# Kernel optimization log

Hardware: AMD Instinct MI355X
Metric: run time of the kernel (lower is better)

The kernel has to match this reference:

```python
import jax, jax.numpy as jnp
import numpy as np

B, L, N, DOUT = 8, 8192, 256, 256  # batch, seq_len, state_dim, output_dim


def setup_inputs() -> dict:
    key = jax.random.key(0)
    k_u, k_h, k_w = jax.random.split(key, 3)
    u = jax.random.normal(k_u, (B, L, 1), dtype=jnp.float32)
    # impulse response buffer (stands in for A_bar^i @ B_bar rows); decay-scaled for realism
    h = jax.random.normal(k_h, (L, N), dtype=jnp.float32) * 0.02
    W = jax.random.normal(k_w, (DOUT, N), dtype=jnp.float32) * (1.0 / np.sqrt(N))
    return {"u": u, "h": h, "W": W}


def reference(u, h, W):
    L_ = h.shape[0]
    n_fft = 2 * L_
    # FFT-based long convolution: U:[B, n_fft//2+1, 1], H:[n_fft//2+1, N]
    U = jnp.fft.rfft(u, n=n_fft, axis=1)
    H = jnp.fft.rfft(h, n=n_fft, axis=0)
    M = U * H[None, :, :]                      # broadcast channel 1 -> N
    m = jnp.fft.irfft(M, n=n_fft, axis=1)[:, :L_, :]  # [B, L, N]
    return jnp.einsum('bln,on->blo', m, W)     # Linear(state_dim -> output_dim), no bias
```

## Files before the change

kernel.cpp:

```cpp
#include <hip/hip_runtime.h>
#include <hip/hip_bf16.h>
#include <stdint.h>
#include <stddef.h>

typedef __attribute__((ext_vector_type(4))) float f32x4;
typedef __attribute__((ext_vector_type(8))) short s16x8;

#define B_    8
#define L_    8192
#define N_    256
#define DOUT_ 256

__device__ __forceinline__ unsigned short f2bf(float f) {
  unsigned int x = __float_as_uint(f);
  x += 0x7fff + ((x >> 16) & 1);
  return (unsigned short)(x >> 16);
}

__global__ void k_convert(const float* __restrict__ h, const float* __restrict__ W,
                          unsigned short* __restrict__ hb, unsigned short* __restrict__ Wb) {
  int t = blockIdx.x * 256 + threadIdx.x;
  int base = t * 4;
  const int TH = L_ * N_;
  const int TW = DOUT_ * N_;
  if (base < TH) {
    float4 v = *(const float4*)(h + base);
    hb[base + 0] = f2bf(v.x); hb[base + 1] = f2bf(v.y);
    hb[base + 2] = f2bf(v.z); hb[base + 3] = f2bf(v.w);
  } else if (base < TH + TW) {
    int wb = base - TH;
    float4 v = *(const float4*)(W + wb);
    Wb[wb + 0] = f2bf(v.x); Wb[wb + 1] = f2bf(v.y);
    Wb[wb + 2] = f2bf(v.z); Wb[wb + 3] = f2bf(v.w);
  }
}

__global__ void k_amat(const float* __restrict__ u, unsigned short* __restrict__ Am) {
  int t = blockIdx.x * 256 + threadIdx.x;
  int i0 = (t & 15) * 8;
  int lp = (t >> 4) & 127;
  int d  = (t >> 11) & 63;
  int b  = t >> 17;
  const float* ub = u + b * L_;
  int base = 128 * d + lp - i0;
  s16x8 v;
#pragma unroll
  for (int j = 0; j < 8; ++j) {
    int idx = base - j;
    float f = (idx >= 0) ? ub[idx] : 0.0f;
    v[j] = (short)f2bf(f);
  }
  *(s16x8*)(Am + (size_t)t * 8) = v;
}

__global__ void k_gt(const unsigned short* __restrict__ Wb, const unsigned short* __restrict__ hb,
                     unsigned short* __restrict__ gT) {
  int gid  = blockIdx.x * 256 + threadIdx.x;
  int lane = gid & 63;
  int wid  = gid >> 6;
  int o_t  = wid >> 7;
  int i_t  = wid & 127;
  int o0 = o_t * 16, i0 = i_t * 64;
  int ln = lane & 15, hi = lane >> 4;
  f32x4 acc[4] = {};
#pragma unroll
  for (int k0 = 0; k0 < N_; k0 += 32) {
    s16x8 a = *(const s16x8*)(Wb + (o0 + ln) * N_ + k0 + 8 * hi);
#pragma unroll
    for (int ns = 0; ns < 4; ++ns) {
      s16x8 bfr = *(const s16x8*)(hb + (i0 + 16 * ns + ln) * N_ + k0 + 8 * hi);
      acc[ns] = __builtin_amdgcn_mfma_f32_16x16x32_bf16(a, bfr, acc[ns], 0, 0, 0);
    }
  }
#pragma unroll
  for (int ns = 0; ns < 4; ++ns)
#pragma unroll
    for (int q = 0; q < 4; ++q)
      gT[(size_t)(o0 + 4 * hi + q) * L_ + i0 + 16 * ns + ln] = f2bf(acc[ns][q]);
}

__global__ __launch_bounds__(256) void k_main(const unsigned short* __restrict__ Am,
                                              const unsigned short* __restrict__ gT,
                                              float* __restrict__ out) {
  __shared__ short Abuf[128 * 64];
  __shared__ short Bbuf[128 * 64];
  const int c = blockIdx.x;
  const int b = blockIdx.y;
  const int r = 63 - blockIdx.z;
  const int t = threadIdx.x;
  const int lane = t & 63;
  const int w = t >> 6;
  const int wm = (w >> 1) * 64, wn = (w & 1) * 64;
  const int ln = lane & 15, hi = lane >> 4;
  const int ob = c * 128;
  const int trow = t >> 3;
  const int tcol = (t & 7) * 8;
  f32x4 acc[4][4] = {};

  const int nkt = 2 * (r + 1);
  for (int kt = 0; kt < nkt; ++kt) {
    const int i0   = kt * 64;
    const int d    = r - (kt >> 1);
    const int ioff = (kt & 1) * 64;
    const unsigned short* Asrc = Am + (((size_t)(b * 64 + d)) << 14) + ioff + tcol;
    const unsigned short* Bsrc = gT + (size_t)(ob + trow) * L_ + i0 + tcol;
#pragma unroll
    for (int call = 0; call < 4; ++call) {
      __builtin_amdgcn_global_load_lds(
          (const __attribute__((address_space(1))) void*)(Asrc + (size_t)(call * 32 + trow) * 128),
          (__attribute__((address_space(3))) void*)(Abuf + call * 2048 + t * 8),
          16, 0, 0);
    }
#pragma unroll
    for (int call = 0; call < 4; ++call) {
      __builtin_amdgcn_global_load_lds(
          (const __attribute__((address_space(1))) void*)(Bsrc + (size_t)(call * 32) * L_),
          (__attribute__((address_space(3))) void*)(Bbuf + call * 2048 + t * 8),
          16, 0, 0);
    }
    __syncthreads();
#pragma unroll
    for (int k0 = 0; k0 < 64; k0 += 32) {
      s16x8 af[4], bfr[4];
#pragma unroll
      for (int m = 0; m < 4; ++m)
        af[m] = *(const s16x8*)(Abuf + (wm + m * 16 + ln) * 64 + k0 + 8 * hi);
#pragma unroll
      for (int n = 0; n < 4; ++n)
        bfr[n] = *(const s16x8*)(Bbuf + (wn + n * 16 + ln) * 64 + k0 + 8 * hi);
#pragma unroll
      for (int m = 0; m < 4; ++m)
#pragma unroll
        for (int n = 0; n < 4; ++n)
          acc[m][n] = __builtin_amdgcn_mfma_f32_16x16x32_bf16(af[m], bfr[n], acc[m][n], 0, 0, 0);
    }
    __syncthreads();
  }

  const int lb = r * 128;
#pragma unroll
  for (int m = 0; m < 4; ++m)
#pragma unroll
    for (int n = 0; n < 4; ++n)
#pragma unroll
      for (int q = 0; q < 4; ++q) {
        int l = lb + wm + m * 16 + 4 * hi + q;
        int o = ob + wn + n * 16 + ln;
        out[(size_t)(b * L_ + l) * DOUT_ + o] = acc[m][n][q];
      }
}

extern "C" void kernel_launch(void* const* d_in, const int* in_sizes, int n_in,
                              void* d_out, int out_size, void* d_ws, size_t ws_size,
                              hipStream_t stream) {
  const float* u = (const float*)d_in[0];
  const float* h = (const float*)d_in[1];
  const float* W = (const float*)d_in[2];
  float* out = (float*)d_out;

  char* ws = (char*)d_ws;
  unsigned short* hb = (unsigned short*)(ws);
  unsigned short* Wb = (unsigned short*)(ws + (size_t)4 * 1024 * 1024);
  unsigned short* gT = (unsigned short*)(ws + (size_t)4 * 1024 * 1024 + 131072);
  unsigned short* Am = (unsigned short*)(ws + (size_t)8 * 1024 * 1024 + 131072);

  k_convert<<<2112, 256, 0, stream>>>(h, W, hb, Wb);
  k_amat<<<4096, 256, 0, stream>>>(u, Am);
  k_gt<<<512, 256, 0, stream>>>(Wb, hb, gT);
  k_main<<<dim3(2, 8, 64), 256, 0, stream>>>(Am, gT, out);
}
```

Measured before the change: 220.4 us.

## Replace Toeplitz GEMM convolution with shared-memory FFT convolution over projected filters

Swaps the dense lower-triangular Toeplitz matmul for an FFT path. The filters are first projected through W (W·hᵀ in bf16), then a 16K-point real FFT runs in LDS as a packed 8K complex FFT for each batch input and each projected filter. One inverse FFT per (batch, output) pair writes the result directly. It also removes the separate conversion and Toeplitz-matrix materialisation kernels by converting fp32 to bf16 inline. This cuts the quadratic MFMA work to O(L log L) per channel. The cost is many LDS-bound radix-2 stages with a barrier each, strided output stores, and extra workspace for twiddles and spectra.

```diff
diff --git a/kernel.cpp b/kernel.cpp
--- a/kernel.cpp
+++ b/kernel.cpp
@@ -10,6 +10,8 @@
 #define L_    8192
 #define N_    256
 #define DOUT_ 256
+#define M_    8192
+#define GSTRIDE 8200
 
 __device__ __forceinline__ unsigned short f2bf(float f) {
   unsigned int x = __float_as_uint(f);
@@ -17,43 +19,19 @@
   return (unsigned short)(x >> 16);
 }
 
-__global__ void k_convert(const float* __restrict__ h, const float* __restrict__ W,
-                          unsigned short* __restrict__ hb, unsigned short* __restrict__ Wb) {
-  int t = blockIdx.x * 256 + threadIdx.x;
-  int base = t * 4;
-  const int TH = L_ * N_;
-  const int TW = DOUT_ * N_;
-  if (base < TH) {
-    float4 v = *(const float4*)(h + base);
-    hb[base + 0] = f2bf(v.x); hb[base + 1] = f2bf(v.y);
-    hb[base + 2] = f2bf(v.z); hb[base + 3] = f2bf(v.w);
-  } else if (base < TH + TW) {
-    int wb = base - TH;
-    float4 v = *(const float4*)(W + wb);
-    Wb[wb + 0] = f2bf(v.x); Wb[wb + 1] = f2bf(v.y);
-    Wb[wb + 2] = f2bf(v.z); Wb[wb + 3] = f2bf(v.w);
-  }
-}
-
-__global__ void k_amat(const float* __restrict__ u, unsigned short* __restrict__ Am) {
-  int t = blockIdx.x * 256 + threadIdx.x;
-  int i0 = (t & 15) * 8;
-  int lp = (t >> 4) & 127;
-  int d  = (t >> 11) & 63;
-  int b  = t >> 17;
-  const float* ub = u + b * L_;
-  int base = 128 * d + lp - i0;
-  s16x8 v;
-#pragma unroll
-  for (int j = 0; j < 8; ++j) {
-    int idx = base - j;
-    float f = (idx >= 0) ? ub[idx] : 0.0f;
-    v[j] = (short)f2bf(f);
-  }
-  *(s16x8*)(Am + (size_t)t * 8) = v;
-}
-
-__global__ void k_gt(const unsigned short* __restrict__ Wb, const unsigned short* __restrict__ hb,
+__device__ __forceinline__ float2 cmul(float2 a, float2 b) {
+  return make_float2(a.x * b.x - a.y * b.y, a.x * b.y + a.y * b.x);
+}
+__device__ __forceinline__ int phi(int i) { return i ^ ((i >> 8) & 7); }
+__device__ __forceinline__ int rev13(int i) { return (int)(__brev((unsigned)i) >> 19); }
+
+__global__ void k_tw(float2* __restrict__ tw) {
+  int k = blockIdx.x * 256 + threadIdx.x;
+  float a = (float)k * 3.8349519697141029e-4f;
+  tw[k] = make_float2(__cosf(a), -__sinf(a));
+}
+
+__global__ void k_gt(const float* __restrict__ W, const float* __restrict__ h,
                      unsigned short* __restrict__ gT) {
   int gid  = blockIdx.x * 256 + threadIdx.x;
   int lane = gid & 63;
@@ -65,11 +43,25 @@
   f32x4 acc[4] = {};
 #pragma unroll
   for (int k0 = 0; k0 < N_; k0 += 32) {
-    s16x8 a = *(const s16x8*)(Wb + (o0 + ln) * N_ + k0 + 8 * hi);
+    const float* wp = W + (o0 + ln) * N_ + k0 + 8 * hi;
+    float4 w0 = *(const float4*)wp;
+    float4 w1 = *(const float4*)(wp + 4);
+    s16x8 a;
+    a[0] = (short)f2bf(w0.x); a[1] = (short)f2bf(w0.y);
+    a[2] = (short)f2bf(w0.z); a[3] = (short)f2bf(w0.w);
+    a[4] = (short)f2bf(w1.x); a[5] = (short)f2bf(w1.y);
+    a[6] = (short)f2bf(w1.z); a[7] = (short)f2bf(w1.w);
 #pragma unroll
     for (int ns = 0; ns < 4; ++ns) {
-      s16x8 bfr = *(const s16x8*)(hb + (i0 + 16 * ns + ln) * N_ + k0 + 8 * hi);
-      acc[ns] = __builtin_amdgcn_mfma_f32_16x16x32_bf16(a, bfr, acc[ns], 0, 0, 0);
+      const float* hp = h + (size_t)(i0 + 16 * ns + ln) * N_ + k0 + 8 * hi;
+      float4 h0 = *(const float4*)hp;
+      float4 h1 = *(const float4*)(hp + 4);
+      s16x8 bb;
+      bb[0] = (short)f2bf(h0.x); bb[1] = (short)f2bf(h0.y);
+      bb[2] = (short)f2bf(h0.z); bb[3] = (short)f2bf(h0.w);
+      bb[4] = (short)f2bf(h1.x); bb[5] = (short)f2bf(h1.y);
+      bb[6] = (short)f2bf(h1.z); bb[7] = (short)f2bf(h1.w);
+      acc[ns] = __builtin_amdgcn_mfma_f32_16x16x32_bf16(a, bb, acc[ns], 0, 0, 0);
     }
   }
 #pragma unroll
@@ -79,75 +71,119 @@
       gT[(size_t)(o0 + 4 * hi + q) * L_ + i0 + 16 * ns + ln] = f2bf(acc[ns][q]);
 }
 
-__global__ __launch_bounds__(256) void k_main(const unsigned short* __restrict__ Am,
-                                              const unsigned short* __restrict__ gT,
-                                              float* __restrict__ out) {
-  __shared__ short Abuf[128 * 64];
-  __shared__ short Bbuf[128 * 64];
-  const int c = blockIdx.x;
-  const int b = blockIdx.y;
-  const int r = 63 - blockIdx.z;
-  const int t = threadIdx.x;
-  const int lane = t & 63;
-  const int w = t >> 6;
-  const int wm = (w >> 1) * 64, wn = (w & 1) * 64;
-  const int ln = lane & 15, hi = lane >> 4;
-  const int ob = c * 128;
-  const int trow = t >> 3;
-  const int tcol = (t & 7) * 8;
-  f32x4 acc[4][4] = {};
-
-  const int nkt = 2 * (r + 1);
-  for (int kt = 0; kt < nkt; ++kt) {
-    const int i0   = kt * 64;
-    const int d    = r - (kt >> 1);
-    const int ioff = (kt & 1) * 64;
-    const unsigned short* Asrc = Am + (((size_t)(b * 64 + d)) << 14) + ioff + tcol;
-    const unsigned short* Bsrc = gT + (size_t)(ob + trow) * L_ + i0 + tcol;
-#pragma unroll
-    for (int call = 0; call < 4; ++call) {
-      __builtin_amdgcn_global_load_lds(
-          (const __attribute__((address_space(1))) void*)(Asrc + (size_t)(call * 32 + trow) * 128),
-          (__attribute__((address_space(3))) void*)(Abuf + call * 2048 + t * 8),
-          16, 0, 0);
-    }
-#pragma unroll
-    for (int call = 0; call < 4; ++call) {
-      __builtin_amdgcn_global_load_lds(
-          (const __attribute__((address_space(1))) void*)(Bsrc + (size_t)(call * 32) * L_),
-          (__attribute__((address_space(3))) void*)(Bbuf + call * 2048 + t * 8),
-          16, 0, 0);
+__device__ __forceinline__ void fft13(float2* zc, const float2* __restrict__ tw,
+                                      int tid, bool inv) {
+  for (int s = 0; s < 13; ++s) {
+    const int sh = 12 - s;
+    const int half = 1 << sh;
+#pragma unroll
+    for (int kp = 0; kp < 8; ++kp) {
+      int j = tid + 512 * kp;
+      int g = j >> sh;
+      int p = j & (half - 1);
+      int i0 = (g << (sh + 1)) + p;
+      int i1 = i0 + half;
+      int a0 = phi(i0), a1 = phi(i1);
+      float2 a = zc[a0];
+      float2 b = zc[a1];
+      float2 w = tw[p << (s + 1)];
+      if (inv) w.y = -w.y;
+      zc[a0] = make_float2(a.x + b.x, a.y + b.y);
+      float2 d = make_float2(a.x - b.x, a.y - b.y);
+      zc[a1] = cmul(d, w);
     }
     __syncthreads();
-#pragma unroll
-    for (int k0 = 0; k0 < 64; k0 += 32) {
-      s16x8 af[4], bfr[4];
-#pragma unroll
-      for (int m = 0; m < 4; ++m)
-        af[m] = *(const s16x8*)(Abuf + (wm + m * 16 + ln) * 64 + k0 + 8 * hi);
-#pragma unroll
-      for (int n = 0; n < 4; ++n)
-        bfr[n] = *(const s16x8*)(Bbuf + (wn + n * 16 + ln) * 64 + k0 + 8 * hi);
-#pragma unroll
-      for (int m = 0; m < 4; ++m)
-#pragma unroll
-        for (int n = 0; n < 4; ++n)
-          acc[m][n] = __builtin_amdgcn_mfma_f32_16x16x32_bf16(af[m], bfr[n], acc[m][n], 0, 0, 0);
-    }
-    __syncthreads();
-  }
-
-  const int lb = r * 128;
-#pragma unroll
-  for (int m = 0; m < 4; ++m)
-#pragma unroll
-    for (int n = 0; n < 4; ++n)
-#pragma unroll
-      for (int q = 0; q < 4; ++q) {
-        int l = lb + wm + m * 16 + 4 * hi + q;
-        int o = ob + wn + n * 16 + ln;
-        out[(size_t)(b * L_ + l) * DOUT_ + o] = acc[m][n][q];
+  }
+}
+
+__global__ __launch_bounds__(512, 4) void k_ffwd(const float* __restrict__ u,
+                                                 const unsigned short* __restrict__ gT,
+                                                 const float2* __restrict__ tw,
+                                                 float2* __restrict__ U,
+                                                 float2* __restrict__ G) {
+  __shared__ float2 zc[M_];
+  const int wg = blockIdx.x;
+  const int tid = threadIdx.x;
+
+  if (wg < 8) {
+    const float2* src = (const float2*)(u + wg * L_);
+#pragma unroll 4
+    for (int kp = 0; kp < 16; ++kp) {
+      int t = tid + 512 * kp;
+      zc[phi(t)] = (t < 4096) ? src[t] : make_float2(0.f, 0.f);
+    }
+  } else {
+    const unsigned int* src = (const unsigned int*)(gT + (size_t)(wg - 8) * L_);
+#pragma unroll 4
+    for (int kp = 0; kp < 16; ++kp) {
+      int t = tid + 512 * kp;
+      float2 v = make_float2(0.f, 0.f);
+      if (t < 4096) {
+        unsigned int pr = src[t];
+        v.x = __uint_as_float(pr << 16);
+        v.y = __uint_as_float(pr & 0xffff0000u);
       }
+      zc[phi(t)] = v;
+    }
+  }
+  __syncthreads();
+
+  fft13(zc, tw, tid, false);
+
+  float2* dst = (wg < 8) ? (U + (size_t)wg * GSTRIDE) : (G + (size_t)(wg - 8) * GSTRIDE);
+#pragma unroll 4
+  for (int kp = 0; kp < 16; ++kp) {
+    int k = tid + 512 * kp;
+    float2 zk  = zc[phi(rev13(k))];
+    float2 zmk = zc[phi(rev13((M_ - k) & (M_ - 1)))];
+    float2 E = make_float2(0.5f * (zk.x + zmk.x), 0.5f * (zk.y - zmk.y));
+    float2 O = make_float2(0.5f * (zk.y + zmk.y), 0.5f * (zmk.x - zk.x));
+    float2 w = tw[k];
+    float2 X = cmul(w, O);
+    dst[k] = make_float2(E.x + X.x, E.y + X.y);
+  }
+  if (tid == 0) {
+    float2 z0 = zc[0];
+    dst[M_] = make_float2(z0.x - z0.y, 0.f);
+  }
+}
+
+__global__ __launch_bounds__(512, 4) void k_conv(const float2* __restrict__ U,
+                                                 const float2* __restrict__ G,
+                                                 const float2* __restrict__ tw,
+                                                 float* __restrict__ out) {
+  __shared__ float2 zc[M_];
+  const int wg = blockIdx.x;
+  const int b = wg >> 8;
+  const int o = wg & 255;
+  const int tid = threadIdx.x;
+  const float2* Ub = U + (size_t)b * GSTRIDE;
+  const float2* Go = G + (size_t)o * GSTRIDE;
+
+#pragma unroll 4
+  for (int kp = 0; kp < 16; ++kp) {
+    int k = tid + 512 * kp;
+    float2 Yk  = cmul(Ub[k], Go[k]);
+    float2 Ymk = cmul(Ub[M_ - k], Go[M_ - k]);
+    float2 E = make_float2(0.5f * (Yk.x + Ymk.x), 0.5f * (Yk.y - Ymk.y));
+    float2 D = make_float2(0.5f * (Yk.x - Ymk.x), 0.5f * (Yk.y + Ymk.y));
+    float2 w = tw[k];
+    float2 O = make_float2(D.x * w.x + D.y * w.y, -D.x * w.y + D.y * w.x);
+    zc[phi(k)] = make_float2(E.x - O.y, E.y + O.x);
+  }
+  __syncthreads();
+
+  fft13(zc, tw, tid, true);
+
+  const float s1 = 1.0f / 8192.0f;
+  float* ob = out + (size_t)b * (L_ * DOUT_) + o;
+#pragma unroll 2
+  for (int kp = 0; kp < 8; ++kp) {
+    int t = tid + 512 * kp;
+    float2 z = zc[phi(rev13(t))];
+    ob[(size_t)(2 * t) * DOUT_]     = z.x * s1;
+    ob[(size_t)(2 * t + 1) * DOUT_] = z.y * s1;
+  }
 }
 
 extern "C" void kernel_launch(void* const* d_in, const int* in_sizes, int n_in,
@@ -159,13 +195,13 @@
   float* out = (float*)d_out;
 
   char* ws = (char*)d_ws;
-  unsigned short* hb = (unsigned short*)(ws);
-  unsigned short* Wb = (unsigned short*)(ws + (size_t)4 * 1024 * 1024);
-  unsigned short* gT = (unsigned short*)(ws + (size_t)4 * 1024 * 1024 + 131072);
-  unsigned short* Am = (unsigned short*)(ws + (size_t)8 * 1024 * 1024 + 131072);
-
-  k_convert<<<2112, 256, 0, stream>>>(h, W, hb, Wb);
-  k_amat<<<4096, 256, 0, stream>>>(u, Am);
-  k_gt<<<512, 256, 0, stream>>>(Wb, hb, gT);
-  k_main<<<dim3(2, 8, 64), 256, 0, stream>>>(Am, gT, out);
-}
+  unsigned short* gT = (unsigned short*)ws;
+  float2* tw = (float2*)(ws + (size_t)4 * 1024 * 1024);
+  float2* U  = (float2*)(ws + (size_t)4 * 1024 * 1024 + 65536);
+  float2* G  = (float2*)(ws + (size_t)4 * 1024 * 1024 + 65536 + 524800);
+
+  k_tw<<<32, 256, 0, stream>>>(tw);
+  k_gt<<<512, 256, 0, stream>>>(W, h, gT);
+  k_ffwd<<<264, 512, 0, stream>>>(u, gT, tw, U, G);
+  k_conv<<<2048, 512, 0, stream>>>(U, G, tw, out);
+}
```

New measurement: 367.7 us. 66.8% more time.
